# Optimization experiments

Hardware: AMD Instinct MI355X
Metric: run time of the kernel (lower is better)

The kernel has to match this reference:

```python
import jax, jax.numpy as jnp
import numpy as np
import math

D_MODEL = 1024
N_HEADS = 16
D_K = D_MODEL // N_HEADS
D_FF = 4096
B, T = 1, 4096
EPS = 1e-5


def _layer_norm(x, g, b):
    mu = jnp.mean(x, axis=-1, keepdims=True)
    var = jnp.mean(jnp.square(x - mu), axis=-1, keepdims=True)
    return (x - mu) * jax.lax.rsqrt(var + EPS) * g + b


def setup_inputs() -> dict:
    key = jax.random.key(0)
    ks = jax.random.split(key, 8)
    s = 0.02
    return {
        "x": jax.random.normal(ks[0], (B, T, D_MODEL), dtype=jnp.float32),
        "ln1_g": jnp.ones((D_MODEL,), jnp.float32),
        "ln1_b": jnp.zeros((D_MODEL,), jnp.float32),
        "w_qkv": jax.random.normal(ks[1], (3 * D_MODEL, D_MODEL), jnp.float32) * s,
        "b_qkv": jnp.zeros((3 * D_MODEL,), jnp.float32),
        "w_out": jax.random.normal(ks[2], (D_MODEL, D_MODEL), jnp.float32) * s,
        "b_out": jnp.zeros((D_MODEL,), jnp.float32),
        "ln2_g": jnp.ones((D_MODEL,), jnp.float32),
        "ln2_b": jnp.zeros((D_MODEL,), jnp.float32),
        "w1": jax.random.normal(ks[3], (D_FF, D_MODEL), jnp.float32) * s,
        "b1": jnp.zeros((D_FF,), jnp.float32),
        "w2": jax.random.normal(ks[4], (D_MODEL, D_FF), jnp.float32) * s,
        "b2": jnp.zeros((D_MODEL,), jnp.float32),
    }


def reference(x, ln1_g, ln1_b, w_qkv, b_qkv, w_out, b_out, ln2_g, ln2_b, w1, b1, w2, b2):
    Bx, Tx, C = x.shape
    # --- attention (pre-norm) ---
    h = _layer_norm(x, ln1_g, ln1_b)
    qkv = h @ w_qkv.T + b_qkv                      # [B,T,3C]
    q, k, v = jnp.split(qkv, 3, axis=-1)
    def heads(t):  # [B,T,C] -> [B,H,T,dk]
        return t.reshape(Bx, Tx, N_HEADS, D_K).transpose(0, 2, 1, 3)
    q, k, v = heads(q), heads(k), heads(v)
    scale = math.sqrt(D_K)
    scores = jnp.einsum("bhqd,bhkd->bhqk", q, k) / scale
    causal = jnp.triu(jnp.ones((Tx, Tx), dtype=bool), k=1)
    scores = jnp.where(causal[None, None], -jnp.inf, scores)
    attn_weights = jax.nn.softmax(scores, axis=-1)  # [B,H,T,T]
    out = jnp.einsum("bhqk,bhkd->bhqd", attn_weights, v)
    out = out.transpose(0, 2, 1, 3).reshape(Bx, Tx, C)
    attn_out = out @ w_out.T + b_out
    x = x + attn_out
    # --- FFN (pre-norm) ---
    h2 = _layer_norm(x, ln2_g, ln2_b)
    ff = jax.nn.gelu(h2 @ w1.T + b1, approximate=False) @ w2.T + b2
    x = x + ff
    return (x, attn_weights)
```

## Files before the change

### kernel.cpp

```cpp
#include <hip/hip_runtime.h>
#include <math.h>

typedef unsigned short u16;
typedef unsigned int u32;
typedef __attribute__((ext_vector_type(8))) short bf16x8;
typedef __attribute__((ext_vector_type(4))) float f32x4;

#define MFMA16(a, b, c) __builtin_amdgcn_mfma_f32_16x16x32_bf16((a), (b), (c), 0, 0, 0)

__device__ __forceinline__ u16 f2bf(float f) {
  u32 u = __float_as_uint(f);
  return (u16)((u + 0x7fffu + ((u >> 16) & 1u)) >> 16);
}

typedef const __attribute__((address_space(1))) u32* gas_t;
typedef __attribute__((address_space(3))) u32* las_t;
__device__ __forceinline__ void gl_lds16(const u16* g, u16* l) {
  __builtin_amdgcn_global_load_lds((gas_t)g, (las_t)l, 16, 0, 0);
}

__global__ __launch_bounds__(256) void cvt_all_kernel(const float* __restrict__ s0, u16* __restrict__ d0,
                                                      const float* __restrict__ s1, u16* __restrict__ d1,
                                                      const float* __restrict__ s2, u16* __restrict__ d2,
                                                      const float* __restrict__ s3, u16* __restrict__ d3) {
  int blk = blockIdx.x, t = threadIdx.x;
  const float* src;
  u16* dst;
  int i;
  if (blk < 3072)      { src = s0; dst = d0; i = blk * 256 + t; }
  else if (blk < 4096) { src = s1; dst = d1; i = (blk - 3072) * 256 + t; }
  else if (blk < 8192) { src = s2; dst = d2; i = (blk - 4096) * 256 + t; }
  else                 { src = s3; dst = d3; i = (blk - 8192) * 256 + t; }
  float4 v = ((const float4*)src)[i];
  ushort4 o;
  o.x = f2bf(v.x); o.y = f2bf(v.y); o.z = f2bf(v.z); o.w = f2bf(v.w);
  ((ushort4*)dst)[i] = o;
}

__global__ __launch_bounds__(256) void ln_kernel(const float* __restrict__ x,
                                                 const float* __restrict__ g,
                                                 const float* __restrict__ b,
                                                 u16* __restrict__ out) {
  int row = blockIdx.x, tid = threadIdx.x;
  float4 v = ((const float4*)(x + (size_t)row * 1024))[tid];
  float s = v.x + v.y + v.z + v.w;
  float s2 = v.x * v.x + v.y * v.y + v.z * v.z + v.w * v.w;
  for (int off = 32; off; off >>= 1) { s += __shfl_xor(s, off); s2 += __shfl_xor(s2, off); }
  __shared__ float ps[4], ps2[4];
  int wave = tid >> 6;
  if ((tid & 63) == 0) { ps[wave] = s; ps2[wave] = s2; }
  __syncthreads();
  float fs = ps[0] + ps[1] + ps[2] + ps[3];
  float fs2 = ps2[0] + ps2[1] + ps2[2] + ps2[3];
  float mu = fs * (1.0f / 1024.0f);
  float var = fs2 * (1.0f / 1024.0f) - mu * mu;
  float rs = rsqrtf(var + 1e-5f);
  float4 gv = ((const float4*)g)[tid];
  float4 bv = ((const float4*)b)[tid];
  ushort4 o;
  o.x = f2bf((v.x - mu) * rs * gv.x + bv.x);
  o.y = f2bf((v.y - mu) * rs * gv.y + bv.y);
  o.z = f2bf((v.z - mu) * rs * gv.z + bv.z);
  o.w = f2bf((v.w - mu) * rs * gv.w + bv.w);
  ((ushort4*)(out + (size_t)row * 1024))[tid] = o;
}

__global__ __launch_bounds__(256) void vtrans_kernel(const u16* __restrict__ qkv,
                                                     u16* __restrict__ vt) {
  const int tt = blockIdx.x, h = blockIdx.y;
  __shared__ u16 tile[64 * 68];
  const int tid = threadIdx.x;
#pragma unroll
  for (int i = 0; i < 2; i++) {
    int c = i * 256 + tid;
    int trow = c >> 3, dc = c & 7;
    const u16* src = qkv + (size_t)(tt * 64 + trow) * 3072 + 2048 + h * 64 + dc * 8;
    uint4 v = *(const uint4*)src;
    *(uint2*)&tile[trow * 68 + dc * 8] = make_uint2(v.x, v.y);
    *(uint2*)&tile[trow * 68 + dc * 8 + 4] = make_uint2(v.z, v.w);
  }
  __syncthreads();
#pragma unroll
  for (int i = 0; i < 2; i++) {
    int c = i * 256 + tid;
    int d = c >> 3, tc = c & 7;
    ushort4 o0, o1;
    o0.x = tile[(tc * 8 + 0) * 68 + d]; o0.y = tile[(tc * 8 + 1) * 68 + d];
    o0.z = tile[(tc * 8 + 2) * 68 + d]; o0.w = tile[(tc * 8 + 3) * 68 + d];
    o1.x = tile[(tc * 8 + 4) * 68 + d]; o1.y = tile[(tc * 8 + 5) * 68 + d];
    o1.z = tile[(tc * 8 + 6) * 68 + d]; o1.w = tile[(tc * 8 + 7) * 68 + d];
    u16* dst = vt + (size_t)(h * 64 + d) * 4096 + tt * 64 + tc * 8;
    *(ushort4*)dst = o0;
    *(ushort4*)(dst + 4) = o1;
  }
}

template <int EPI>
__device__ __forceinline__ void gemm_body(const u16* __restrict__ A, const u16* __restrict__ B,
                                          const float* __restrict__ bias,
                                          const float* __restrict__ resid,
                                          void* __restrict__ Cout, int M, int N, int K,
                                          int bxi, int byi, u16* As, u16* Bs) {
  const int tid = threadIdx.x, lane = tid & 63, wave = tid >> 6;
  const int wr = wave >> 1, wc = wave & 1;
  const int bm = byi * 128, bn = bxi * 128;
  const int r = lane & 15, qd = lane >> 4;
  (void)M;

  const u16 *ag[2], *bg[2];
  u16 *al[2], *bl[2];
#pragma unroll
  for (int i = 0; i < 2; i++) {
    int C0 = wave * 128 + i * 64;
    int sc = C0 + lane;
    int row = sc >> 2;
    int q = (sc & 3) ^ ((row >> 1) & 3);
    ag[i] = A + (size_t)(bm + row) * K + q * 8;
    al[i] = &As[C0 * 8];
    bg[i] = B + (size_t)(bn + row) * K + q * 8;
    bl[i] = &Bs[C0 * 8];
  }
  const int swz = (r >> 1) & 3;
  f32x4 acc[4][4] = {};
  for (int k0 = 0; k0 < K; k0 += 32) {
#pragma unroll
    for (int i = 0; i < 2; i++) { gl_lds16(ag[i] + k0, al[i]); gl_lds16(bg[i] + k0, bl[i]); }
    __syncthreads();
    bf16x8 af[4], bfr[4];
#pragma unroll
    for (int mi = 0; mi < 4; mi++) {
      int row = wr * 64 + mi * 16 + r;
      af[mi] = *(const bf16x8*)&As[(row * 4 + (qd ^ swz)) * 8];
    }
#pragma unroll
    for (int ni = 0; ni < 4; ni++) {
      int row = wc * 64 + ni * 16 + r;
      bfr[ni] = *(const bf16x8*)&Bs[(row * 4 + (qd ^ swz)) * 8];
    }
#pragma unroll
    for (int mi = 0; mi < 4; mi++)
#pragma unroll
      for (int ni = 0; ni < 4; ni++)
        acc[mi][ni] = MFMA16(af[mi], bfr[ni], acc[mi][ni]);
    __syncthreads();
  }
  const int crow0 = bm + wr * 64 + qd * 4;
  const int ccol0 = bn + wc * 64 + r;
#pragma unroll
  for (int ni = 0; ni < 4; ni++) {
    int col = ccol0 + ni * 16;
    float bv = bias[col];
#pragma unroll
    for (int mi = 0; mi < 4; mi++) {
#pragma unroll
      for (int rg = 0; rg < 4; rg++) {
        int row = crow0 + mi * 16 + rg;
        float v = acc[mi][ni][rg] + bv;
        if (EPI == 1) v += resid[(size_t)row * N + col];
        if (EPI == 2) v = 0.5f * v * (1.0f + erff(v * 0.70710678118654752f));
        if (EPI == 1) ((float*)Cout)[(size_t)row * N + col] = v;
        else ((u16*)Cout)[(size_t)row * N + col] = f2bf(v);
      }
    }
  }
}

template <int EPI>
__global__ __launch_bounds__(256, 2) void gemm_bf16(const u16* __restrict__ A,
                                                    const u16* __restrict__ B,
                                                    const float* __restrict__ bias,
                                                    const float* __restrict__ resid,
                                                    void* __restrict__ Cout,
                                                    int M, int N, int K) {
  __shared__ u16 As[128 * 32];
  __shared__ u16 Bs[128 * 32];
  gemm_body<EPI>(A, B, bias, resid, Cout, M, N, K, blockIdx.x, blockIdx.y, As, Bs);
}

__global__ __launch_bounds__(256, 2) void attn_pass1(const u16* __restrict__ qkv,
                                                     const u16* __restrict__ vt,
                                                     u16* __restrict__ aout,
                                                     float* __restrict__ mstat,
                                                     float* __restrict__ lstat) {
  const int b = blockIdx.x;
  int h, qb;
  if (b < 256) { h = b >> 4; qb = b & 15; }
  else         { int b2 = b - 256; h = b2 >> 4; qb = 31 - (b2 & 15); }
  const int tid = threadIdx.x, lane = tid & 63, wave = tid >> 6;
  const int r = lane & 15, qd = lane >> 4;
  __shared__ u16 Qs[128 * 64];
  __shared__ u16 Ks[128 * 64];
  __shared__ u16 Vts[64 * 128];
  __shared__ u16 Ps[128 * 128];

#pragma unroll
  for (int i = 0; i < 4; i++) {
    int C0 = wave * 256 + i * 64;
    int sc = C0 + lane;
    int row = sc >> 3;
    int q = (sc & 7) ^ (row & 7);
    gl_lds16(qkv + (size_t)(qb * 128 + row) * 3072 + h * 64 + q * 8, &Qs[C0 * 8]);
  }
  const u16 *kg[4], *vg[4];
  u16 *kl[4], *vl[4];
#pragma unroll
  for (int i = 0; i < 4; i++) {
    int C0 = wave * 256 + i * 64;
    int sc = C0 + lane;
    int row = sc >> 3;
    int q = (sc & 7) ^ (row & 7);
    kg[i] = qkv + (size_t)row * 3072 + 1024 + h * 64 + q * 8;
    kl[i] = &Ks[C0 * 8];
    int d = sc >> 4;
    int qq = (sc & 15) ^ (d & 15);
    vg[i] = vt + (size_t)(h * 64 + d) * 4096 + qq * 8;
    vl[i] = &Vts[C0 * 8];
  }
  __syncthreads();
  bf16x8 qf[2][2];
#pragma unroll
  for (int ni = 0; ni < 2; ni++)
#pragma unroll
    for (int kk = 0; kk < 2; kk++) {
      int qrow = wave * 32 + ni * 16 + r;
      int qq = kk * 4 + qd;
      qf[ni][kk] = *(const bf16x8*)&Qs[(qrow * 8 + (qq ^ (qrow & 7))) * 8];
    }
  f32x4 ot[4][2] = {};
  float m_run[2] = {-INFINITY, -INFINITY};
  float l_run[2] = {0.f, 0.f};

  for (int kb = 0; kb <= qb; kb++) {
#pragma unroll
    for (int i = 0; i < 4; i++) {
      gl_lds16(kg[i] + (size_t)kb * 128 * 3072, kl[i]);
      gl_lds16(vg[i] + kb * 128, vl[i]);
    }
    __syncthreads();
    f32x4 st[8][2] = {};
#pragma unroll
    for (int kk = 0; kk < 2; kk++) {
      bf16x8 kf[8];
#pragma unroll
      for (int mi = 0; mi < 8; mi++) {
        int krow = mi * 16 + r;
        int qq = kk * 4 + qd;
        kf[mi] = *(const bf16x8*)&Ks[(krow * 8 + (qq ^ (krow & 7))) * 8];
      }
#pragma unroll
      for (int mi = 0; mi < 8; mi++)
#pragma unroll
        for (int ni = 0; ni < 2; ni++)
          st[mi][ni] = MFMA16(kf[mi], qf[ni][kk], st[mi][ni]);
    }
    if (kb == qb) {
#pragma unroll
      for (int mi = 0; mi < 8; mi++) {
        int k0 = mi * 16 + qd * 4;
#pragma unroll
        for (int ni = 0; ni < 2; ni++) {
          int qloc = wave * 32 + ni * 16 + r;
#pragma unroll
          for (int rg = 0; rg < 4; rg++)
            if (k0 + rg > qloc) st[mi][ni][rg] = -INFINITY;
        }
      }
    }
    float mb[2], alpha[2];
#pragma unroll
    for (int ni = 0; ni < 2; ni++) {
      float mx = -INFINITY;
#pragma unroll
      for (int mi = 0; mi < 8; mi++)
        mx = fmaxf(mx, fmaxf(fmaxf(st[mi][ni][0], st[mi][ni][1]),
                             fmaxf(st[mi][ni][2], st[mi][ni][3])));
      mx = fmaxf(mx, __shfl_xor(mx, 16));
      mx = fmaxf(mx, __shfl_xor(mx, 32));
      float mn = fmaxf(m_run[ni], mx);
      alpha[ni] = __expf((m_run[ni] - mn) * 0.125f);
      m_run[ni] = mn;
      mb[ni] = mn;
    }
#pragma unroll
    for (int ni = 0; ni < 2; ni++) {
      int qrow = wave * 32 + ni * 16 + r;
      float ls = 0.f;
#pragma unroll
      for (int mi = 0; mi < 8; mi++) {
        float p0 = __expf((st[mi][ni][0] - mb[ni]) * 0.125f);
        float p1 = __expf((st[mi][ni][1] - mb[ni]) * 0.125f);
        float p2 = __expf((st[mi][ni][2] - mb[ni]) * 0.125f);
        float p3 = __expf((st[mi][ni][3] - mb[ni]) * 0.125f);
        ls += p0 + p1 + p2 + p3;
        ushort4 pk;
        pk.x = f2bf(p0); pk.y = f2bf(p1); pk.z = f2bf(p2); pk.w = f2bf(p3);
        int qq = mi * 2 + (qd >> 1);
        int sc = qrow * 16 + (qq ^ (qrow & 15));
        *(ushort4*)&Ps[sc * 8 + (qd & 1) * 4] = pk;
      }
      ls += __shfl_xor(ls, 16);
      ls += __shfl_xor(ls, 32);
      l_run[ni] = l_run[ni] * alpha[ni] + ls;
#pragma unroll
      for (int mi = 0; mi < 4; mi++) ot[mi][ni] = ot[mi][ni] * alpha[ni];
    }
    __syncthreads();
#pragma unroll
    for (int kk = 0; kk < 4; kk++) {
      bf16x8 vf[4], pf[2];
#pragma unroll
      for (int mi = 0; mi < 4; mi++) {
        int d = mi * 16 + r;
        int qq = kk * 4 + qd;
        vf[mi] = *(const bf16x8*)&Vts[(d * 16 + (qq ^ (d & 15))) * 8];
      }
#pragma unroll
      for (int ni = 0; ni < 2; ni++) {
        int qrow = wave * 32 + ni * 16 + r;
        int qq = kk * 4 + qd;
        pf[ni] = *(const bf16x8*)&Ps[(qrow * 16 + (qq ^ (qrow & 15))) * 8];
      }
#pragma unroll
      for (int mi = 0; mi < 4; mi++)
#pragma unroll
        for (int ni = 0; ni < 2; ni++)
          ot[mi][ni] = MFMA16(vf[mi], pf[ni], ot[mi][ni]);
    }
    __syncthreads();
  }
#pragma unroll
  for (int ni = 0; ni < 2; ni++) {
    float il = 1.0f / l_run[ni];
    int qg = qb * 128 + wave * 32 + ni * 16 + r;
    if (qd == 0) {
      mstat[h * 4096 + qg] = m_run[ni];
      lstat[h * 4096 + qg] = l_run[ni];
    }
#pragma unroll
    for (int mi = 0; mi < 4; mi++) {
      ushort4 o;
      o.x = f2bf(ot[mi][ni][0] * il);
      o.y = f2bf(ot[mi][ni][1] * il);
      o.z = f2bf(ot[mi][ni][2] * il);
      o.w = f2bf(ot[mi][ni][3] * il);
      *(ushort4*)&aout[(size_t)qg * 1024 + h * 64 + mi * 16 + qd * 4] = o;
    }
  }
}

__device__ __forceinline__ void pass2_body(const u16* __restrict__ qkv,
                                           const float* __restrict__ mstat,
                                           const float* __restrict__ lstat,
                                           float* __restrict__ attn, int qb, int h,
                                           u16* Qs, u16* Ks) {
  const int tid = threadIdx.x, lane = tid & 63, wave = tid >> 6;
  const int r = lane & 15, qd = lane >> 4;
#pragma unroll
  for (int i = 0; i < 4; i++) {
    int C0 = wave * 256 + i * 64;
    int sc = C0 + lane;
    int row = sc >> 3;
    int q = (sc & 7) ^ (row & 7);
    gl_lds16(qkv + (size_t)(qb * 128 + row) * 3072 + h * 64 + q * 8, &Qs[C0 * 8]);
  }
  const u16* kg[4];
  u16* kl[4];
#pragma unroll
  for (int i = 0; i < 4; i++) {
    int C0 = wave * 256 + i * 64;
    int sc = C0 + lane;
    int row = sc >> 3;
    int q = (sc & 7) ^ (row & 7);
    kg[i] = qkv + (size_t)row * 3072 + 1024 + h * 64 + q * 8;
    kl[i] = &Ks[C0 * 8];
  }
  __syncthreads();
  bf16x8 qf[2][2];
  float mrow[2], ilrow[2];
#pragma unroll
  for (int ni = 0; ni < 2; ni++) {
#pragma unroll
    for (int kk = 0; kk < 2; kk++) {
      int qrow = wave * 32 + ni * 16 + r;
      int qq = kk * 4 + qd;
      qf[ni][kk] = *(const bf16x8*)&Qs[(qrow * 8 + (qq ^ (qrow & 7))) * 8];
    }
    int qg = qb * 128 + wave * 32 + ni * 16 + r;
    mrow[ni] = mstat[h * 4096 + qg];
    ilrow[ni] = 1.0f / lstat[h * 4096 + qg];
  }
  float* ahead = attn + ((size_t)h << 24);
  for (int kb = 0; kb < 32; kb++) {
    if (kb <= qb) {
#pragma unroll
      for (int i = 0; i < 4; i++) gl_lds16(kg[i] + (size_t)kb * 128 * 3072, kl[i]);
      __syncthreads();
      f32x4 st[8][2] = {};
#pragma unroll
      for (int kk = 0; kk < 2; kk++) {
        bf16x8 kf[8];
#pragma unroll
        for (int mi = 0; mi < 8; mi++) {
          int krow = mi * 16 + r;
          int qq = kk * 4 + qd;
          kf[mi] = *(const bf16x8*)&Ks[(krow * 8 + (qq ^ (krow & 7))) * 8];
        }
#pragma unroll
        for (int mi = 0; mi < 8; mi++)
#pragma unroll
          for (int ni = 0; ni < 2; ni++)
            st[mi][ni] = MFMA16(kf[mi], qf[ni][kk], st[mi][ni]);
      }
#pragma unroll
      for (int ni = 0; ni < 2; ni++) {
        int qloc = wave * 32 + ni * 16 + r;
        size_t rowbase = (size_t)(qb * 128 + qloc) * 4096 + (size_t)kb * 128;
#pragma unroll
        for (int mi = 0; mi < 8; mi++) {
          int k0 = mi * 16 + qd * 4;
          float v0, v1, v2, v3;
          v0 = __expf((st[mi][ni][0] - mrow[ni]) * 0.125f) * ilrow[ni];
          v1 = __expf((st[mi][ni][1] - mrow[ni]) * 0.125f) * ilrow[ni];
          v2 = __expf((st[mi][ni][2] - mrow[ni]) * 0.125f) * ilrow[ni];
          v3 = __expf((st[mi][ni][3] - mrow[ni]) * 0.125f) * ilrow[ni];
          if (kb == qb) {
            if (k0 + 0 > qloc) v0 = 0.f;
            if (k0 + 1 > qloc) v1 = 0.f;
            if (k0 + 2 > qloc) v2 = 0.f;
            if (k0 + 3 > qloc) v3 = 0.f;
          }
          *(float4*)(ahead + rowbase + k0) = make_float4(v0, v1, v2, v3);
        }
      }
      __syncthreads();
    } else {
      size_t base = (size_t)(qb * 128) * 4096 + (size_t)kb * 128;
      float4 z = make_float4(0.f, 0.f, 0.f, 0.f);
#pragma unroll
      for (int i = 0; i < 16; i++) {
        int idx = i * 256 + tid;
        int ql = idx >> 5;
        int ko = (idx & 31) * 4;
        *(float4*)(ahead + base + (size_t)ql * 4096 + ko) = z;
      }
    }
  }
}

template <int EPI, int NXB, int GPG, int PPG, int PBASE>
__global__ __launch_bounds__(256, 2) void gemm_pass2_fused(
    const u16* __restrict__ A, const u16* __restrict__ B, const float* __restrict__ bias,
    const float* __restrict__ resid, void* __restrict__ Cout, int M, int N, int K,
    const u16* __restrict__ qkv, const float* __restrict__ mstat,
    const float* __restrict__ lstat, float* __restrict__ attn) {
  __shared__ u16 smem[128 * 64 * 2];
  constexpr int GRP = GPG + PPG;
  int idx = blockIdx.x;
  int grp = idx / GRP, r = idx - grp * GRP;
  if (r < GPG) {
    int g = grp * GPG + r;
    gemm_body<EPI>(A, B, bias, resid, Cout, M, N, K, g % NXB, g / NXB, smem, smem + 128 * 32);
  } else {
    int p = PBASE + grp * PPG + (r - GPG);
    pass2_body(qkv, mstat, lstat, attn, p & 31, p >> 5, smem, smem + 128 * 64);
  }
}

extern "C" void kernel_launch(void* const* d_in, const int* in_sizes, int n_in,
                              void* d_out, int out_size, void* d_ws, size_t ws_size,
                              hipStream_t stream) {
  const float* x     = (const float*)d_in[0];
  const float* ln1_g = (const float*)d_in[1];
  const float* ln1_b = (const float*)d_in[2];
  const float* w_qkv = (const float*)d_in[3];
  const float* b_qkv = (const float*)d_in[4];
  const float* w_out = (const float*)d_in[5];
  const float* b_out = (const float*)d_in[6];
  const float* ln2_g = (const float*)d_in[7];
  const float* ln2_b = (const float*)d_in[8];
  const float* w1    = (const float*)d_in[9];
  const float* b1    = (const float*)d_in[10];
  const float* w2    = (const float*)d_in[11];
  const float* b2    = (const float*)d_in[12];
  float* out_x = (float*)d_out;
  float* out_attn = out_x + (size_t)4096 * 1024;

  char* ws = (char*)d_ws;
  size_t off = 0;
  auto alloc = [&](size_t bytes) {
    void* p = ws + off;
    off += (bytes + 255) & ~(size_t)255;
    return p;
  };
  u16* WQKV = (u16*)alloc((size_t)3072 * 1024 * 2);
  u16* WOUT = (u16*)alloc((size_t)1024 * 1024 * 2);
  u16* W1   = (u16*)alloc((size_t)4096 * 1024 * 2);
  u16* W2   = (u16*)alloc((size_t)1024 * 4096 * 2);
  u16* H1   = (u16*)alloc((size_t)8388608);
  u16* QKV  = (u16*)alloc((size_t)25165824);
  u16* FF   = (u16*)alloc((size_t)33554432);
  u16* VT   = (u16*)alloc((size_t)8388608);
  float* MST = (float*)alloc((size_t)262144);
  float* LST = (float*)alloc((size_t)262144);
  u16* AOUT = (u16*)alloc((size_t)8388608);
  float* X1 = (float*)alloc((size_t)16777216);
  u16* H2  = (u16*)alloc((size_t)8388608);
  (void)ws_size; (void)in_sizes; (void)n_in; (void)out_size;

  cvt_all_kernel<<<12288, 256, 0, stream>>>(w_qkv, WQKV, w_out, WOUT, w1, W1, w2, W2);
  ln_kernel<<<4096, 256, 0, stream>>>(x, ln1_g, ln1_b, H1);
  gemm_bf16<0><<<dim3(24, 32), 256, 0, stream>>>(H1, WQKV, b_qkv, nullptr, QKV, 4096, 3072, 1024);
  vtrans_kernel<<<dim3(64, 16), 256, 0, stream>>>(QKV, VT);
  attn_pass1<<<512, 256, 0, stream>>>(QKV, VT, AOUT, MST, LST);
  gemm_pass2_fused<1, 8, 2, 1, 0><<<384, 256, 0, stream>>>(
      AOUT, WOUT, b_out, x, X1, 4096, 1024, 1024, QKV, MST, LST, out_attn);
  ln_kernel<<<4096, 256, 0, stream>>>(X1, ln2_g, ln2_b, H2);
  gemm_pass2_fused<2, 32, 16, 3, 128><<<1216, 256, 0, stream>>>(
      H2, W1, b1, nullptr, FF, 4096, 4096, 1024, QKV, MST, LST, out_attn);
  gemm_pass2_fused<1, 8, 4, 3, 320><<<448, 256, 0, stream>>>(
      FF, W2, b2, X1, out_x, 4096, 1024, 4096, QKV, MST, LST, out_attn);
}
```

Measured before the change: 1.663 ms.

## Prefetch K via registers in attention pass1 and split pass2 into key-block chunks

```diff
diff --git a/kernel.cpp b/kernel.cpp
--- a/kernel.cpp
+++ b/kernel.cpp
@@ -201,22 +201,32 @@
     int q = (sc & 7) ^ (row & 7);
     gl_lds16(qkv + (size_t)(qb * 128 + row) * 3072 + h * 64 + q * 8, &Qs[C0 * 8]);
   }
-  const u16 *kg[4], *vg[4];
-  u16 *kl[4], *vl[4];
+  const u16* kgb[4];
+  u16* klds[4];
+#pragma unroll
+  for (int i = 0; i < 4; i++) {
+    int g = i * 256 + tid;
+    int row = g >> 3, qq = g & 7;
+    kgb[i] = qkv + (size_t)row * 3072 + 1024 + h * 64 + qq * 8;
+    klds[i] = &Ks[(row * 8 + (qq ^ (row & 7))) * 8];
+  }
+  const u16* vg[4];
+  u16* vl[4];
 #pragma unroll
   for (int i = 0; i < 4; i++) {
     int C0 = wave * 256 + i * 64;
     int sc = C0 + lane;
-    int row = sc >> 3;
-    int q = (sc & 7) ^ (row & 7);
-    kg[i] = qkv + (size_t)row * 3072 + 1024 + h * 64 + q * 8;
-    kl[i] = &Ks[C0 * 8];
     int d = sc >> 4;
     int qq = (sc & 15) ^ (d & 15);
     vg[i] = vt + (size_t)(h * 64 + d) * 4096 + qq * 8;
     vl[i] = &Vts[C0 * 8];
   }
-  __syncthreads();
+  uint4 kcur[4], knxt[4] = {};
+#pragma unroll
+  for (int i = 0; i < 4; i++) kcur[i] = *(const uint4*)kgb[i];
+  asm volatile("s_waitcnt vmcnt(0) lgkmcnt(0)" ::: "memory");
+  __builtin_amdgcn_s_barrier();
+
   bf16x8 qf[2][2];
 #pragma unroll
   for (int ni = 0; ni < 2; ni++)
@@ -232,11 +242,16 @@
 
   for (int kb = 0; kb <= qb; kb++) {
 #pragma unroll
-    for (int i = 0; i < 4; i++) {
-      gl_lds16(kg[i] + (size_t)kb * 128 * 3072, kl[i]);
-      gl_lds16(vg[i] + kb * 128, vl[i]);
-    }
-    __syncthreads();
+    for (int i = 0; i < 4; i++) *(uint4*)klds[i] = kcur[i];
+#pragma unroll
+    for (int i = 0; i < 4; i++) gl_lds16(vg[i] + kb * 128, vl[i]);
+    __builtin_amdgcn_sched_barrier(0);
+    if (kb < qb) {
+#pragma unroll
+      for (int i = 0; i < 4; i++) knxt[i] = *(const uint4*)(kgb[i] + (size_t)(kb + 1) * 393216);
+    }
+    asm volatile("s_waitcnt lgkmcnt(0)" ::: "memory");
+    __builtin_amdgcn_s_barrier();
     f32x4 st[8][2] = {};
 #pragma unroll
     for (int kk = 0; kk < 2; kk++) {
@@ -304,7 +319,9 @@
 #pragma unroll
       for (int mi = 0; mi < 4; mi++) ot[mi][ni] = ot[mi][ni] * alpha[ni];
     }
-    __syncthreads();
+    if (kb < qb) asm volatile("s_waitcnt vmcnt(4) lgkmcnt(0)" ::: "memory");
+    else         asm volatile("s_waitcnt vmcnt(0) lgkmcnt(0)" ::: "memory");
+    __builtin_amdgcn_s_barrier();
 #pragma unroll
     for (int kk = 0; kk < 4; kk++) {
       bf16x8 vf[4], pf[2];
@@ -326,7 +343,12 @@
         for (int ni = 0; ni < 2; ni++)
           ot[mi][ni] = MFMA16(vf[mi], pf[ni], ot[mi][ni]);
     }
-    __syncthreads();
+    asm volatile("s_waitcnt lgkmcnt(0)" ::: "memory");
+    __builtin_amdgcn_s_barrier();
+    if (kb < qb) {
+#pragma unroll
+      for (int i = 0; i < 4; i++) kcur[i] = knxt[i];
+    }
   }
 #pragma unroll
   for (int ni = 0; ni < 2; ni++) {
@@ -351,46 +373,49 @@
 __device__ __forceinline__ void pass2_body(const u16* __restrict__ qkv,
                                            const float* __restrict__ mstat,
                                            const float* __restrict__ lstat,
-                                           float* __restrict__ attn, int qb, int h,
+                                           float* __restrict__ attn, int qb, int h, int k0,
                                            u16* Qs, u16* Ks) {
   const int tid = threadIdx.x, lane = tid & 63, wave = tid >> 6;
   const int r = lane & 15, qd = lane >> 4;
-#pragma unroll
-  for (int i = 0; i < 4; i++) {
-    int C0 = wave * 256 + i * 64;
-    int sc = C0 + lane;
-    int row = sc >> 3;
-    int q = (sc & 7) ^ (row & 7);
-    gl_lds16(qkv + (size_t)(qb * 128 + row) * 3072 + h * 64 + q * 8, &Qs[C0 * 8]);
-  }
+  const bool has_compute = (k0 <= qb);
+  bf16x8 qf[2][2];
+  float mrow[2], ilrow[2];
   const u16* kg[4];
   u16* kl[4];
-#pragma unroll
-  for (int i = 0; i < 4; i++) {
-    int C0 = wave * 256 + i * 64;
-    int sc = C0 + lane;
-    int row = sc >> 3;
-    int q = (sc & 7) ^ (row & 7);
-    kg[i] = qkv + (size_t)row * 3072 + 1024 + h * 64 + q * 8;
-    kl[i] = &Ks[C0 * 8];
-  }
-  __syncthreads();
-  bf16x8 qf[2][2];
-  float mrow[2], ilrow[2];
-#pragma unroll
-  for (int ni = 0; ni < 2; ni++) {
-#pragma unroll
-    for (int kk = 0; kk < 2; kk++) {
-      int qrow = wave * 32 + ni * 16 + r;
-      int qq = kk * 4 + qd;
-      qf[ni][kk] = *(const bf16x8*)&Qs[(qrow * 8 + (qq ^ (qrow & 7))) * 8];
-    }
-    int qg = qb * 128 + wave * 32 + ni * 16 + r;
-    mrow[ni] = mstat[h * 4096 + qg];
-    ilrow[ni] = 1.0f / lstat[h * 4096 + qg];
+  if (has_compute) {
+#pragma unroll
+    for (int i = 0; i < 4; i++) {
+      int C0 = wave * 256 + i * 64;
+      int sc = C0 + lane;
+      int row = sc >> 3;
+      int q = (sc & 7) ^ (row & 7);
+      gl_lds16(qkv + (size_t)(qb * 128 + row) * 3072 + h * 64 + q * 8, &Qs[C0 * 8]);
+    }
+#pragma unroll
+    for (int i = 0; i < 4; i++) {
+      int C0 = wave * 256 + i * 64;
+      int sc = C0 + lane;
+      int row = sc >> 3;
+      int q = (sc & 7) ^ (row & 7);
+      kg[i] = qkv + (size_t)row * 3072 + 1024 + h * 64 + q * 8;
+      kl[i] = &Ks[C0 * 8];
+    }
+    __syncthreads();
+#pragma unroll
+    for (int ni = 0; ni < 2; ni++) {
+#pragma unroll
+      for (int kk = 0; kk < 2; kk++) {
+        int qrow = wave * 32 + ni * 16 + r;
+        int qq = kk * 4 + qd;
+        qf[ni][kk] = *(const bf16x8*)&Qs[(qrow * 8 + (qq ^ (qrow & 7))) * 8];
+      }
+      int qg = qb * 128 + wave * 32 + ni * 16 + r;
+      mrow[ni] = mstat[h * 4096 + qg];
+      ilrow[ni] = 1.0f / lstat[h * 4096 + qg];
+    }
   }
   float* ahead = attn + ((size_t)h << 24);
-  for (int kb = 0; kb < 32; kb++) {
+  for (int kb = k0; kb < k0 + 8; kb++) {
     if (kb <= qb) {
 #pragma unroll
       for (int i = 0; i < 4; i++) gl_lds16(kg[i] + (size_t)kb * 128 * 3072, kl[i]);
@@ -417,19 +442,19 @@
         size_t rowbase = (size_t)(qb * 128 + qloc) * 4096 + (size_t)kb * 128;
 #pragma unroll
         for (int mi = 0; mi < 8; mi++) {
-          int k0 = mi * 16 + qd * 4;
+          int kk0 = mi * 16 + qd * 4;
           float v0, v1, v2, v3;
           v0 = __expf((st[mi][ni][0] - mrow[ni]) * 0.125f) * ilrow[ni];
           v1 = __expf((st[mi][ni][1] - mrow[ni]) * 0.125f) * ilrow[ni];
           v2 = __expf((st[mi][ni][2] - mrow[ni]) * 0.125f) * ilrow[ni];
           v3 = __expf((st[mi][ni][3] - mrow[ni]) * 0.125f) * ilrow[ni];
           if (kb == qb) {
-            if (k0 + 0 > qloc) v0 = 0.f;
-            if (k0 + 1 > qloc) v1 = 0.f;
-            if (k0 + 2 > qloc) v2 = 0.f;
-            if (k0 + 3 > qloc) v3 = 0.f;
+            if (kk0 + 0 > qloc) v0 = 0.f;
+            if (kk0 + 1 > qloc) v1 = 0.f;
+            if (kk0 + 2 > qloc) v2 = 0.f;
+            if (kk0 + 3 > qloc) v3 = 0.f;
           }
-          *(float4*)(ahead + rowbase + k0) = make_float4(v0, v1, v2, v3);
+          *(float4*)(ahead + rowbase + kk0) = make_float4(v0, v1, v2, v3);
         }
       }
       __syncthreads();
@@ -456,13 +481,14 @@
   __shared__ u16 smem[128 * 64 * 2];
   constexpr int GRP = GPG + PPG;
   int idx = blockIdx.x;
-  int grp = idx / GRP, r = idx - grp * GRP;
-  if (r < GPG) {
-    int g = grp * GPG + r;
+  int grp = idx / GRP, rr = idx - grp * GRP;
+  if (rr < GPG) {
+    int g = grp * GPG + rr;
     gemm_body<EPI>(A, B, bias, resid, Cout, M, N, K, g % NXB, g / NXB, smem, smem + 128 * 32);
   } else {
-    int p = PBASE + grp * PPG + (r - GPG);
-    pass2_body(qkv, mstat, lstat, attn, p & 31, p >> 5, smem, smem + 128 * 64);
+    int p = PBASE + grp * PPG + (rr - GPG);
+    pass2_body(qkv, mstat, lstat, attn, p & 31, (p >> 5) & 15, (p >> 9) * 8,
+               smem, smem + 128 * 64);
   }
 }
 
@@ -512,11 +538,10 @@
   gemm_bf16<0><<<dim3(24, 32), 256, 0, stream>>>(H1, WQKV, b_qkv, nullptr, QKV, 4096, 3072, 1024);
   vtrans_kernel<<<dim3(64, 16), 256, 0, stream>>>(QKV, VT);
   attn_pass1<<<512, 256, 0, stream>>>(QKV, VT, AOUT, MST, LST);
-  gemm_pass2_fused<1, 8, 2, 1, 0><<<384, 256, 0, stream>>>(
-      AOUT, WOUT, b_out, x, X1, 4096, 1024, 1024, QKV, MST, LST, out_attn);
+  gemm_bf16<1><<<dim3(8, 32), 256, 0, stream>>>(AOUT, WOUT, b_out, x, X1, 4096, 1024, 1024);
   ln_kernel<<<4096, 256, 0, stream>>>(X1, ln2_g, ln2_b, H2);
-  gemm_pass2_fused<2, 32, 16, 3, 128><<<1216, 256, 0, stream>>>(
+  gemm_pass2_fused<2, 32, 2, 1, 0><<<1536, 256, 0, stream>>>(
       H2, W1, b1, nullptr, FF, 4096, 4096, 1024, QKV, MST, LST, out_attn);
-  gemm_pass2_fused<1, 8, 4, 3, 320><<<448, 256, 0, stream>>>(
+  gemm_pass2_fused<1, 8, 1, 6, 512><<<1792, 256, 0, stream>>>(
       FF, W2, b2, X1, out_x, 4096, 1024, 4096, QKV, MST, LST, out_attn);
 }
```

After: 1.589 ms. 1.05x faster.
